# Optimization experiments

Hardware: AMD Instinct MI355X
Metric: run time of the kernel (lower is better)

The kernel has to match this reference:

```python
import jax, jax.numpy as jnp
import numpy as np

B, T, C_FEAT, H = 1024, 256, 512, 256


def setup_inputs() -> dict:
    key = jax.random.key(0)
    ks = jax.random.split(key, 8)
    s_ih = 1.0 / np.sqrt(H)
    return {
        "features": jax.random.normal(ks[0], (B, T, C_FEAT), dtype=jnp.float32),
        "last_coord": jax.random.normal(ks[1], (B, 2), dtype=jnp.float32),
        "W_ih": jax.random.uniform(ks[2], (3 * H, C_FEAT + 2), jnp.float32, -s_ih, s_ih),
        "W_hh": jax.random.uniform(ks[3], (3 * H, H), jnp.float32, -s_ih, s_ih),
        "b_ih": jax.random.uniform(ks[4], (3 * H,), jnp.float32, -s_ih, s_ih),
        "b_hh": jax.random.uniform(ks[5], (3 * H,), jnp.float32, -s_ih, s_ih),
        "W_proj": jax.random.uniform(ks[6], (2, H), jnp.float32, -s_ih, s_ih),
        "b_proj": jax.random.uniform(ks[7], (2,), jnp.float32, -s_ih, s_ih),
    }


def reference(features, last_coord, W_ih, W_hh, b_ih, b_hh, W_proj, b_proj):
    # features: (B, T, C_feat); last_coord: (B, 2)
    Bb, Tt, Cf = features.shape
    Hh = W_hh.shape[1]
    h0 = jnp.zeros((Bb, Hh), dtype=features.dtype)

    def step(carry, feat_t):
        h, coord = carry
        x = jnp.concatenate([feat_t, coord], axis=1)          # (B, C+2)
        gi = x @ W_ih.T + b_ih                                 # (B, 3H)
        gh = h @ W_hh.T + b_hh                                 # (B, 3H)
        i_r, i_z, i_n = jnp.split(gi, 3, axis=1)
        h_r, h_z, h_n = jnp.split(gh, 3, axis=1)
        r = jax.nn.sigmoid(i_r + h_r)
        z = jax.nn.sigmoid(i_z + h_z)
        n = jnp.tanh(i_n + r * h_n)
        h_new = (1.0 - z) * n + z * h                          # PyTorch GRU update
        disp = h_new @ W_proj.T + b_proj                       # (B, 2)
        return (h_new, coord + disp), disp

    feats_t = jnp.swapaxes(features, 0, 1)                     # (T, B, C)
    _, disps = jax.lax.scan(step, (h0, last_coord), feats_t)   # (T, B, 2)
    return jnp.swapaxes(disps, 0, 1)                           # (B, T, 2)
```

## Files before the change

### kernel.cpp

```cpp
#include <hip/hip_runtime.h>
#include <stdint.h>

typedef unsigned short u16;
typedef unsigned int   u32;
typedef __attribute__((ext_vector_type(8))) __bf16 bf16x8;
typedef __attribute__((ext_vector_type(4))) float  f32x4;
typedef __attribute__((ext_vector_type(8))) u16    u16x8;
typedef __attribute__((ext_vector_type(4))) u16    u16x4;
typedef __attribute__((ext_vector_type(2))) u32    u32x2;
typedef __attribute__((ext_vector_type(2))) float  f32x2;

__device__ __forceinline__ u16 f2bf(float f) {
    u32 u = __float_as_uint(f);
    u32 r = (u + 0x7fffu + ((u >> 16) & 1u)) >> 16;
    return (u16)r;
}
__device__ __forceinline__ float bf2f(u16 v) { return __uint_as_float(((u32)v) << 16); }
__device__ __forceinline__ bf16x8 as_bf(u16x8 x) { union { u16x8 a; bf16x8 b; } u; u.a = x; return u.b; }
__device__ __forceinline__ void gload_lds16(const void* g, void* l) {
    __builtin_amdgcn_global_load_lds((const __attribute__((address_space(1))) void*)g,
                                     (__attribute__((address_space(3))) void*)l, 16, 0, 0);
}

__global__ void k_prep(const float* __restrict__ W_ih, const float* __restrict__ W_hh,
                       const float* __restrict__ b_ih, const float* __restrict__ b_hh,
                       u16* __restrict__ Wf, u16* __restrict__ Whh, float* __restrict__ bsum) {
    int i = blockIdx.x * 256 + threadIdx.x;
    if (i < 768 * 512) { int o = i >> 9, k = i & 511; Wf[i] = f2bf(W_ih[o * 514 + k]); }
    if (i < 768 * 256) { Whh[i] = f2bf(W_hh[i]); }
    if (i < 768)       { bsum[i] = b_ih[i] + (i < 512 ? b_hh[i] : 0.f); }
}

__global__ void k_cast(const float* __restrict__ f, u16* __restrict__ o) {
    const size_t N8 = (size_t)262144 * 512 / 8;
    for (size_t i = (size_t)blockIdx.x * 256 + threadIdx.x; i < N8; i += (size_t)gridDim.x * 256) {
        float4 a = ((const float4*)f)[i * 2];
        float4 b = ((const float4*)f)[i * 2 + 1];
        u16x8 v;
        v[0] = f2bf(a.x); v[1] = f2bf(a.y); v[2] = f2bf(a.z); v[3] = f2bf(a.w);
        v[4] = f2bf(b.x); v[5] = f2bf(b.y); v[6] = f2bf(b.z); v[7] = f2bf(b.w);
        ((u16x8*)o)[i] = v;
    }
}

__device__ __forceinline__ void xcd_remap(int& n0, int& m0) {
    int phys = blockIdx.x + blockIdx.y * 6;
    int logical = (phys & 7) * 1536 + (phys >> 3);
    n0 = (logical % 6) * 128;
    m0 = (logical / 6) * 128;
}

__global__ __launch_bounds__(256) void k_gemm(const u16* __restrict__ featbf,
                                              const u16* __restrict__ Wf,
                                              const float* __restrict__ bsum,
                                              float* __restrict__ Gf) {
    __shared__ u16 As[128 * 64];
    __shared__ u16 Bs[128 * 64];
    const int tid = threadIdx.x;
    const int l = tid & 63, wv = tid >> 6;
    const int wr = wv >> 1, wc = wv & 1;
    const int lb = l & 15, lq = l >> 4;
    int n0, m0; xcd_remap(n0, m0);
    const int rl = l >> 3;
    const int c16 = (l & 7) * 16;
    const int sswz = (rl & 7) << 4;

    f32x4 acc[4][4] = {};

    for (int k0 = 0; k0 < 512; k0 += 64) {
        __syncthreads();
#pragma unroll
        for (int i = 0; i < 4; ++i) {
            int ci = wv * 4 + i;
            int r = ci * 8 + rl;
            const char* sa = (const char*)(featbf + (size_t)(m0 + r) * 512) + k0 * 2 + (c16 ^ sswz);
            gload_lds16(sa, (char*)As + ci * 1024);
            const char* sb = (const char*)(Wf + (size_t)(n0 + r) * 512) + k0 * 2 + (c16 ^ sswz);
            gload_lds16(sb, (char*)Bs + ci * 1024);
        }
        __syncthreads();
#pragma unroll
        for (int kc = 0; kc < 2; ++kc) {
            bf16x8 af[4], bfr[4];
#pragma unroll
            for (int mi = 0; mi < 4; ++mi) {
                int row = wr * 64 + mi * 16 + lb;
                af[mi] = *(const bf16x8*)((char*)As + row * 128 + (((kc * 32 + lq * 8) * 2) ^ ((row & 7) << 4)));
            }
#pragma unroll
            for (int ni = 0; ni < 4; ++ni) {
                int row = wc * 64 + ni * 16 + lb;
                bfr[ni] = *(const bf16x8*)((char*)Bs + row * 128 + (((kc * 32 + lq * 8) * 2) ^ ((row & 7) << 4)));
            }
#pragma unroll
            for (int mi = 0; mi < 4; ++mi)
#pragma unroll
                for (int ni = 0; ni < 4; ++ni)
                    acc[mi][ni] = __builtin_amdgcn_mfma_f32_16x16x32_bf16(af[mi], bfr[ni], acc[mi][ni], 0, 0, 0);
        }
    }
#pragma unroll
    for (int ni = 0; ni < 4; ++ni) {
        int o = n0 + wc * 64 + ni * 16 + lb;
        float bi = bsum[o];
#pragma unroll
        for (int mi = 0; mi < 4; ++mi) {
#pragma unroll
            for (int j = 0; j < 4; ++j) {
                int m = m0 + wr * 64 + mi * 16 + lq * 4 + j;
                int bb = m >> 8, tt = m & 255;
                Gf[(size_t)((tt << 10) + bb) * 768 + o] = acc[mi][ni][j] + bi;
            }
        }
    }
}

template<typename ST>
__global__ __launch_bounds__(256) void k_gemm_legacy(const float* __restrict__ feat,
                                                     const u16* __restrict__ Wf,
                                                     const float* __restrict__ bsum,
                                                     ST* __restrict__ Gf) {
    __shared__ u16 As[128 * 64];
    __shared__ u16 Bs[128 * 64];
    const int tid = threadIdx.x;
    const int l = tid & 63, wv = tid >> 6;
    const int wr = wv >> 1, wc = wv & 1;
    const int lb = l & 15, lq = l >> 4;
    int n0, m0; xcd_remap(n0, m0);
    const int srow = tid >> 1, scol = (tid & 1) * 32;

    f32x4 acc[4][4] = {};

    for (int k0 = 0; k0 < 512; k0 += 64) {
        __syncthreads();
        const float* ga = feat + (size_t)(m0 + srow) * 512 + k0 + scol;
        const u16*   gb = Wf + (n0 + srow) * 512 + k0 + scol;
        char* arow = (char*)As + srow * 128;
        char* brow = (char*)Bs + srow * 128;
        const int swz = (srow & 7) << 4;
#pragma unroll
        for (int i = 0; i < 4; ++i) {
            float4 f0 = *(const float4*)(ga + i * 8);
            float4 f1 = *(const float4*)(ga + i * 8 + 4);
            u16x8 v;
            v[0] = f2bf(f0.x); v[1] = f2bf(f0.y); v[2] = f2bf(f0.z); v[3] = f2bf(f0.w);
            v[4] = f2bf(f1.x); v[5] = f2bf(f1.y); v[6] = f2bf(f1.z); v[7] = f2bf(f1.w);
            *(u16x8*)(arow + (((scol + i * 8) * 2) ^ swz)) = v;
            u16x8 w8 = *(const u16x8*)(gb + i * 8);
            *(u16x8*)(brow + (((scol + i * 8) * 2) ^ swz)) = w8;
        }
        __syncthreads();
#pragma unroll
        for (int kc = 0; kc < 2; ++kc) {
            bf16x8 af[4], bfr[4];
#pragma unroll
            for (int mi = 0; mi < 4; ++mi) {
                int row = wr * 64 + mi * 16 + lb;
                af[mi] = *(const bf16x8*)((char*)As + row * 128 + (((kc * 32 + lq * 8) * 2) ^ ((row & 7) << 4)));
            }
#pragma unroll
            for (int ni = 0; ni < 4; ++ni) {
                int row = wc * 64 + ni * 16 + lb;
                bfr[ni] = *(const bf16x8*)((char*)Bs + row * 128 + (((kc * 32 + lq * 8) * 2) ^ ((row & 7) << 4)));
            }
#pragma unroll
            for (int mi = 0; mi < 4; ++mi)
#pragma unroll
                for (int ni = 0; ni < 4; ++ni)
                    acc[mi][ni] = __builtin_amdgcn_mfma_f32_16x16x32_bf16(af[mi], bfr[ni], acc[mi][ni], 0, 0, 0);
        }
    }
#pragma unroll
    for (int ni = 0; ni < 4; ++ni) {
        int o = n0 + wc * 64 + ni * 16 + lb;
        float bi = bsum[o];
#pragma unroll
        for (int mi = 0; mi < 4; ++mi) {
#pragma unroll
            for (int j = 0; j < 4; ++j) {
                int m = m0 + wr * 64 + mi * 16 + lq * 4 + j;
                int bb = m >> 8, tt = m & 255;
                size_t idx = (size_t)((tt << 10) + bb) * 768 + o;
                float v = acc[mi][ni][j] + bi;
                if constexpr (sizeof(ST) == 4) Gf[idx] = v; else Gf[idx] = f2bf(v);
            }
        }
    }
}

template<typename ST>
__global__ __launch_bounds__(512, 2) void k_rnn(const float* __restrict__ lastc,
                                                const float* __restrict__ W_ih,
                                                const float* __restrict__ bhh_g,
                                                const float* __restrict__ Wp,
                                                const float* __restrict__ bp,
                                                const u16* __restrict__ Whh,
                                                const ST* __restrict__ Gf,
                                                float* __restrict__ out) {
    __shared__ u16 Wlds[144 * 512];
    __shared__ u16 hbf[16 * 320];
    __shared__ float wpL[256 * 2];
    __shared__ float coordL[16 * 2];
    __shared__ float dPart[8 * 16 * 2];

    const int tid = threadIdx.x, l = tid & 63, wv = tid >> 6;
    const int lb = l & 15, lq = l >> 4;
    const int bb = blockIdx.x << 4;
    const int swz = (lb & 7) << 4;

    bf16x8 wres[5][3][2];
    bf16x8 wcf[3][2];
    float bhhn[2][4];
#pragma unroll
    for (int g = 0; g < 3; ++g)
#pragma unroll
        for (int ut = 0; ut < 2; ++ut) {
            int row = g * 256 + (2 * wv + ut) * 16 + lb;
#pragma unroll
            for (int kc = 0; kc < 5; ++kc)
                wres[kc][g][ut] = *(const bf16x8*)(Whh + row * 256 + kc * 32 + lq * 8);
            u16x8 cf = {0, 0, 0, 0, 0, 0, 0, 0};
            if (lq == 0) {
                cf[0] = f2bf(W_ih[row * 514 + 512]);
                cf[1] = f2bf(W_ih[row * 514 + 513]);
            }
            wcf[g][ut] = as_bf(cf);
        }
#pragma unroll
    for (int ut = 0; ut < 2; ++ut)
#pragma unroll
        for (int j = 0; j < 4; ++j)
            bhhn[ut][j] = bhh_g[512 + (2 * wv + ut) * 16 + lq * 4 + j];

    for (int i = tid; i < 36864; i += 512) {
        int s = i >> 8, r = i & 255, ll = r >> 2, e2 = r & 3;
        int g = s / 48, rem = s - g * 48, tt = rem / 3, kcs = rem - tt * 3;
        int row = g * 256 + tt * 16 + (ll & 15);
        int k = (5 + kcs) * 32 + (ll >> 4) * 8 + e2 * 2;
        ((u32*)Wlds)[i] = *(const u32*)(Whh + row * 256 + k);
    }
    for (int i = tid; i < 16 * 320 / 2; i += 512) ((u32*)hbf)[i] = 0u;
    if (tid < 256) { wpL[tid * 2] = Wp[tid]; wpL[tid * 2 + 1] = Wp[256 + tid]; }
    float bpc = (tid < 32) ? bp[tid & 1] : 0.f;
    __syncthreads();
    if (tid < 32) {
        int b = tid >> 1, c = tid & 1;
        float cc = lastc[(bb + b) * 2 + c];
        coordL[b * 2 + c] = cc;
        *(u16*)((char*)hbf + b * 640 + 512 + ((c * 2) ^ ((b & 7) << 4))) = f2bf(cc);
    }
    __syncthreads();

    float hreg[2][4] = {};
    float prevD = 0.f;
    const ST* gr = Gf + (size_t)(bb + lb) * 768 + lq * 4;
    const char* hrow = (const char*)hbf + lb * 640;

    for (int t = 0; t < 256; ++t) {
        if (t > 0 && tid < 32)
            out[((size_t)(bb + (tid >> 1)) * 256 + (t - 1)) * 2 + (tid & 1)] = prevD;

        float gf[3][2][4];
#pragma unroll
        for (int g = 0; g < 3; ++g)
#pragma unroll
            for (int ut = 0; ut < 2; ++ut) {
                int off = g * 256 + (2 * wv + ut) * 16;
                if constexpr (sizeof(ST) == 4) {
                    float4 v = *(const float4*)(gr + off);
                    gf[g][ut][0] = v.x; gf[g][ut][1] = v.y; gf[g][ut][2] = v.z; gf[g][ut][3] = v.w;
                } else {
                    u16x4 v = *(const u16x4*)(gr + off);
#pragma unroll
                    for (int j = 0; j < 4; ++j) gf[g][ut][j] = bf2f(v[j]);
                }
            }

        f32x4 acc[3][2] = {};
        f32x4 accC[2] = {};
#pragma unroll
        for (int kc = 0; kc < 5; ++kc) {
            bf16x8 hb = *(const bf16x8*)(hrow + ((kc * 64 + lq * 16) ^ swz));
#pragma unroll
            for (int g = 0; g < 3; ++g)
#pragma unroll
                for (int ut = 0; ut < 2; ++ut)
                    acc[g][ut] = __builtin_amdgcn_mfma_f32_16x16x32_bf16(wres[kc][g][ut], hb, acc[g][ut], 0, 0, 0);
        }
#pragma unroll
        for (int kcs = 0; kcs < 3; ++kcs) {
            bf16x8 hb = *(const bf16x8*)(hrow + (((5 + kcs) * 64 + lq * 16) ^ swz));
#pragma unroll
            for (int g = 0; g < 3; ++g)
#pragma unroll
                for (int ut = 0; ut < 2; ++ut) {
                    int s = (g * 16 + 2 * wv + ut) * 3 + kcs;
                    bf16x8 wl = *(const bf16x8*)((const char*)Wlds + s * 1024 + l * 16);
                    acc[g][ut] = __builtin_amdgcn_mfma_f32_16x16x32_bf16(wl, hb, acc[g][ut], 0, 0, 0);
                }
        }
        {
            bf16x8 hbE = *(const bf16x8*)(hrow + 512 + ((lq * 16) ^ swz));
#pragma unroll
            for (int ut = 0; ut < 2; ++ut) {
                acc[0][ut] = __builtin_amdgcn_mfma_f32_16x16x32_bf16(wcf[0][ut], hbE, acc[0][ut], 0, 0, 0);
                acc[1][ut] = __builtin_amdgcn_mfma_f32_16x16x32_bf16(wcf[1][ut], hbE, acc[1][ut], 0, 0, 0);
                accC[ut]   = __builtin_amdgcn_mfma_f32_16x16x32_bf16(wcf[2][ut], hbE, accC[ut],   0, 0, 0);
            }
        }
        __syncthreads();

        float pd0 = 0.f, pd1 = 0.f;
#pragma unroll
        for (int ut = 0; ut < 2; ++ut) {
            int ub = (2 * wv + ut) * 16 + lq * 4;
            float4 wpa = *(const float4*)(wpL + ub * 2);
            float4 wpb = *(const float4*)(wpL + ub * 2 + 4);
            u16 hpk[4];
#pragma unroll
            for (int j = 0; j < 4; ++j) {
                float r = 1.f / (1.f + __expf(-(gf[0][ut][j] + acc[0][ut][j])));
                float z = 1.f / (1.f + __expf(-(gf[1][ut][j] + acc[1][ut][j])));
                float ghn = acc[2][ut][j] + bhhn[ut][j];
                float xn = gf[2][ut][j] + accC[ut][j] + r * ghn;
                float e = __expf(-2.f * fabsf(xn));
                float th = (1.f - e) / (1.f + e);
                th = (xn >= 0.f) ? th : -th;
                float hn = (1.f - z) * th + z * hreg[ut][j];
                hreg[ut][j] = hn;
                float w0 = (j == 0) ? wpa.x : (j == 1) ? wpa.z : (j == 2) ? wpb.x : wpb.z;
                float w1 = (j == 0) ? wpa.y : (j == 1) ? wpa.w : (j == 2) ? wpb.y : wpb.w;
                pd0 += w0 * hn;
                pd1 += w1 * hn;
                hpk[j] = f2bf(hn);
            }
            u32x2 pv;
            pv.x = (u32)hpk[0] | ((u32)hpk[1] << 16);
            pv.y = (u32)hpk[2] | ((u32)hpk[3] << 16);
            *(u32x2*)((char*)hbf + lb * 640 + ((ub * 2) ^ swz)) = pv;
        }
        pd0 += __shfl_xor(pd0, 16); pd0 += __shfl_xor(pd0, 32);
        pd1 += __shfl_xor(pd1, 16); pd1 += __shfl_xor(pd1, 32);
        if (l < 16) { dPart[(wv * 16 + l) * 2] = pd0; dPart[(wv * 16 + l) * 2 + 1] = pd1; }
        __syncthreads();

        if (tid < 32) {
            int b = tid >> 1, c = tid & 1;
            float d = bpc;
#pragma unroll
            for (int w8 = 0; w8 < 8; ++w8) d += dPart[(w8 * 16 + b) * 2 + c];
            prevD = d;
            float nc = coordL[b * 2 + c] + d;
            coordL[b * 2 + c] = nc;
            *(u16*)((char*)hbf + b * 640 + 512 + ((c * 2) ^ ((b & 7) << 4))) = f2bf(nc);
        }
        __syncthreads();
        gr += (size_t)1024 * 768;
    }
    if (tid < 32)
        out[((size_t)(bb + (tid >> 1)) * 256 + 255) * 2 + (tid & 1)] = prevD;
}

extern "C" void kernel_launch(void* const* d_in, const int* in_sizes, int n_in,
                              void* d_out, int out_size, void* d_ws, size_t ws_size,
                              hipStream_t stream) {
    const float* feat   = (const float*)d_in[0];
    const float* lastc  = (const float*)d_in[1];
    const float* W_ih   = (const float*)d_in[2];
    const float* W_hh   = (const float*)d_in[3];
    const float* b_ih   = (const float*)d_in[4];
    const float* b_hh   = (const float*)d_in[5];
    const float* W_proj = (const float*)d_in[6];
    const float* b_proj = (const float*)d_in[7];
    float* out = (float*)d_out;

    char* ws = (char*)d_ws;
    u16*   Wf    = (u16*)ws;
    u16*   Whh   = (u16*)(ws + 786432);
    float* bsum  = (float*)(ws + 786432 + 393216);
    const size_t off_fb = 786432 + 393216 + 3072;
    u16*   featbf = (u16*)(ws + off_fb);
    const size_t off_gf_full = off_fb + (size_t)262144 * 512 * 2;
    const size_t need_full  = off_gf_full + (size_t)262144 * 768 * 4;
    const size_t need_tier2 = off_fb + (size_t)262144 * 768 * 4;

    k_prep<<<1536, 256, 0, stream>>>(W_ih, W_hh, b_ih, b_hh, Wf, Whh, bsum);

    if (ws_size >= need_full) {
        float* Gf = (float*)(ws + off_gf_full);
        k_cast<<<16384, 256, 0, stream>>>(feat, featbf);
        k_gemm<<<dim3(6, 2048), 256, 0, stream>>>(featbf, Wf, bsum, Gf);
        k_rnn<float><<<64, 512, 0, stream>>>(lastc, W_ih, b_hh, W_proj, b_proj, Whh, Gf, out);
    } else if (ws_size >= need_tier2) {
        float* Gf = (float*)(ws + off_fb);
        k_gemm_legacy<float><<<dim3(6, 2048), 256, 0, stream>>>(feat, Wf, bsum, Gf);
        k_rnn<float><<<64, 512, 0, stream>>>(lastc, W_ih, b_hh, W_proj, b_proj, Whh, Gf, out);
    } else {
        u16* Gf = (u16*)(ws + off_fb);
        k_gemm_legacy<u16><<<dim3(6, 2048), 256, 0, stream>>>(feat, Wf, bsum, Gf);
        k_rnn<u16><<<64, 512, 0, stream>>>(lastc, W_ih, b_hh, W_proj, b_proj, Whh, Gf, out);
    }
}
```

Measured before the change: 1.511 ms.

## Double RNN block to 16 waves, split weights across regs/LDS/global, stage gates via LDS

The recurrent kernel now runs 1024 threads (16 waves) per block, so each wave owns one 16-unit tile per gate instead of two. This halves the per-wave MFMA chain on the serial timestep path. W_hh k-chunks 0-4 stay in registers, chunks 6-7 move to LDS, and chunk 5 is re-read from global/L2 every step. Precomputed input gates are prefetched into LDS with async global_load_lds at the start of each step, hiding load latency behind the MFMAs. The cost is heavier barriers across 16 waves, a larger projection reduction, and an extra global weight load per step.

```diff
diff --git a/kernel.cpp b/kernel.cpp
--- a/kernel.cpp
+++ b/kernel.cpp
@@ -8,7 +8,6 @@
 typedef __attribute__((ext_vector_type(8))) u16    u16x8;
 typedef __attribute__((ext_vector_type(4))) u16    u16x4;
 typedef __attribute__((ext_vector_type(2))) u32    u32x2;
-typedef __attribute__((ext_vector_type(2))) float  f32x2;
 
 __device__ __forceinline__ u16 f2bf(float f) {
     u32 u = __float_as_uint(f);
@@ -189,57 +188,54 @@
 }
 
 template<typename ST>
-__global__ __launch_bounds__(512, 2) void k_rnn(const float* __restrict__ lastc,
-                                                const float* __restrict__ W_ih,
-                                                const float* __restrict__ bhh_g,
-                                                const float* __restrict__ Wp,
-                                                const float* __restrict__ bp,
-                                                const u16* __restrict__ Whh,
-                                                const ST* __restrict__ Gf,
-                                                float* __restrict__ out) {
-    __shared__ u16 Wlds[144 * 512];
+__global__ __launch_bounds__(1024, 4) void k_rnn(const float* __restrict__ lastc,
+                                                 const float* __restrict__ W_ih,
+                                                 const float* __restrict__ bhh_g,
+                                                 const float* __restrict__ Wp,
+                                                 const float* __restrict__ bp,
+                                                 const u16* __restrict__ Whh,
+                                                 const ST* __restrict__ Gf,
+                                                 float* __restrict__ out) {
+    __shared__ u16 Wlds[96 * 512];
+    __shared__ __align__(16) char GfL[16 * 3120];
     __shared__ u16 hbf[16 * 320];
     __shared__ float wpL[256 * 2];
     __shared__ float coordL[16 * 2];
-    __shared__ float dPart[8 * 16 * 2];
+    __shared__ float dPart[16 * 16 * 2];
 
     const int tid = threadIdx.x, l = tid & 63, wv = tid >> 6;
     const int lb = l & 15, lq = l >> 4;
     const int bb = blockIdx.x << 4;
     const int swz = (lb & 7) << 4;
 
-    bf16x8 wres[5][3][2];
-    bf16x8 wcf[3][2];
-    float bhhn[2][4];
-#pragma unroll
-    for (int g = 0; g < 3; ++g)
-#pragma unroll
-        for (int ut = 0; ut < 2; ++ut) {
-            int row = g * 256 + (2 * wv + ut) * 16 + lb;
-#pragma unroll
-            for (int kc = 0; kc < 5; ++kc)
-                wres[kc][g][ut] = *(const bf16x8*)(Whh + row * 256 + kc * 32 + lq * 8);
-            u16x8 cf = {0, 0, 0, 0, 0, 0, 0, 0};
-            if (lq == 0) {
-                cf[0] = f2bf(W_ih[row * 514 + 512]);
-                cf[1] = f2bf(W_ih[row * 514 + 513]);
-            }
-            wcf[g][ut] = as_bf(cf);
-        }
-#pragma unroll
-    for (int ut = 0; ut < 2; ++ut)
-#pragma unroll
-        for (int j = 0; j < 4; ++j)
-            bhhn[ut][j] = bhh_g[512 + (2 * wv + ut) * 16 + lq * 4 + j];
-
-    for (int i = tid; i < 36864; i += 512) {
+    bf16x8 wres[5][3];
+    bf16x8 wcf[3];
+    float bhhn[4];
+#pragma unroll
+    for (int g = 0; g < 3; ++g) {
+        int row = g * 256 + wv * 16 + lb;
+#pragma unroll
+        for (int kc = 0; kc < 5; ++kc)
+            wres[kc][g] = *(const bf16x8*)(Whh + row * 256 + kc * 32 + lq * 8);
+        u16x8 cf = {0, 0, 0, 0, 0, 0, 0, 0};
+        if (lq == 0) {
+            cf[0] = f2bf(W_ih[row * 514 + 512]);
+            cf[1] = f2bf(W_ih[row * 514 + 513]);
+        }
+        wcf[g] = as_bf(cf);
+    }
+#pragma unroll
+    for (int j = 0; j < 4; ++j)
+        bhhn[j] = bhh_g[512 + wv * 16 + lq * 4 + j];
+
+    for (int i = tid; i < 24576; i += 1024) {
         int s = i >> 8, r = i & 255, ll = r >> 2, e2 = r & 3;
-        int g = s / 48, rem = s - g * 48, tt = rem / 3, kcs = rem - tt * 3;
-        int row = g * 256 + tt * 16 + (ll & 15);
-        int k = (5 + kcs) * 32 + (ll >> 4) * 8 + e2 * 2;
+        int g = s >> 5, rem = s & 31, tt2 = rem >> 1, kcs = rem & 1;
+        int row = g * 256 + tt2 * 16 + (ll & 15);
+        int k = (6 + kcs) * 32 + (ll >> 4) * 8 + e2 * 2;
         ((u32*)Wlds)[i] = *(const u32*)(Whh + row * 256 + k);
     }
-    for (int i = tid; i < 16 * 320 / 2; i += 512) ((u32*)hbf)[i] = 0u;
+    for (int i = tid; i < 2560; i += 1024) ((u32*)hbf)[i] = 0u;
     if (tid < 256) { wpL[tid * 2] = Wp[tid]; wpL[tid * 2 + 1] = Wp[256 + tid]; }
     float bpc = (tid < 32) ? bp[tid & 1] : 0.f;
     __syncthreads();
@@ -251,89 +247,98 @@
     }
     __syncthreads();
 
-    float hreg[2][4] = {};
+    float hreg[4] = {};
     float prevD = 0.f;
-    const ST* gr = Gf + (size_t)(bb + lb) * 768 + lq * 4;
     const char* hrow = (const char*)hbf + lb * 640;
+    const u16* w5base = Whh + (size_t)(wv * 16 + lb) * 256 + 160 + lq * 8;
 
     for (int t = 0; t < 256; ++t) {
         if (t > 0 && tid < 32)
             out[((size_t)(bb + (tid >> 1)) * 256 + (t - 1)) * 2 + (tid & 1)] = prevD;
 
-        float gf[3][2][4];
+        if constexpr (sizeof(ST) == 4) {
+            const char* gsrc = (const char*)Gf + (size_t)t * 3145728 + (size_t)(bb + wv) * 3072;
+#pragma unroll
+            for (int i = 0; i < 3; ++i)
+                gload_lds16(gsrc + i * 1024 + l * 16, GfL + wv * 3120 + i * 1024);
+        }
+        bf16x8 w5[3];
 #pragma unroll
         for (int g = 0; g < 3; ++g)
-#pragma unroll
-            for (int ut = 0; ut < 2; ++ut) {
-                int off = g * 256 + (2 * wv + ut) * 16;
-                if constexpr (sizeof(ST) == 4) {
-                    float4 v = *(const float4*)(gr + off);
-                    gf[g][ut][0] = v.x; gf[g][ut][1] = v.y; gf[g][ut][2] = v.z; gf[g][ut][3] = v.w;
-                } else {
-                    u16x4 v = *(const u16x4*)(gr + off);
-#pragma unroll
-                    for (int j = 0; j < 4; ++j) gf[g][ut][j] = bf2f(v[j]);
-                }
-            }
-
-        f32x4 acc[3][2] = {};
-        f32x4 accC[2] = {};
+            w5[g] = *(const bf16x8*)(w5base + g * 65536);
+
+        f32x4 acc[3] = {};
+        f32x4 accC = {};
 #pragma unroll
         for (int kc = 0; kc < 5; ++kc) {
             bf16x8 hb = *(const bf16x8*)(hrow + ((kc * 64 + lq * 16) ^ swz));
 #pragma unroll
             for (int g = 0; g < 3; ++g)
-#pragma unroll
-                for (int ut = 0; ut < 2; ++ut)
-                    acc[g][ut] = __builtin_amdgcn_mfma_f32_16x16x32_bf16(wres[kc][g][ut], hb, acc[g][ut], 0, 0, 0);
-        }
-#pragma unroll
-        for (int kcs = 0; kcs < 3; ++kcs) {
-            bf16x8 hb = *(const bf16x8*)(hrow + (((5 + kcs) * 64 + lq * 16) ^ swz));
+                acc[g] = __builtin_amdgcn_mfma_f32_16x16x32_bf16(wres[kc][g], hb, acc[g], 0, 0, 0);
+        }
+#pragma unroll
+        for (int kcs = 0; kcs < 2; ++kcs) {
+            bf16x8 hb = *(const bf16x8*)(hrow + (((6 + kcs) * 64 + lq * 16) ^ swz));
+#pragma unroll
+            for (int g = 0; g < 3; ++g) {
+                int s = (g * 16 + wv) * 2 + kcs;
+                bf16x8 wl = *(const bf16x8*)((const char*)Wlds + s * 1024 + l * 16);
+                acc[g] = __builtin_amdgcn_mfma_f32_16x16x32_bf16(wl, hb, acc[g], 0, 0, 0);
+            }
+        }
+        {
+            bf16x8 hb5 = *(const bf16x8*)(hrow + ((5 * 64 + lq * 16) ^ swz));
 #pragma unroll
             for (int g = 0; g < 3; ++g)
-#pragma unroll
-                for (int ut = 0; ut < 2; ++ut) {
-                    int s = (g * 16 + 2 * wv + ut) * 3 + kcs;
-                    bf16x8 wl = *(const bf16x8*)((const char*)Wlds + s * 1024 + l * 16);
-                    acc[g][ut] = __builtin_amdgcn_mfma_f32_16x16x32_bf16(wl, hb, acc[g][ut], 0, 0, 0);
-                }
+                acc[g] = __builtin_amdgcn_mfma_f32_16x16x32_bf16(w5[g], hb5, acc[g], 0, 0, 0);
         }
         {
             bf16x8 hbE = *(const bf16x8*)(hrow + 512 + ((lq * 16) ^ swz));
-#pragma unroll
-            for (int ut = 0; ut < 2; ++ut) {
-                acc[0][ut] = __builtin_amdgcn_mfma_f32_16x16x32_bf16(wcf[0][ut], hbE, acc[0][ut], 0, 0, 0);
-                acc[1][ut] = __builtin_amdgcn_mfma_f32_16x16x32_bf16(wcf[1][ut], hbE, acc[1][ut], 0, 0, 0);
-                accC[ut]   = __builtin_amdgcn_mfma_f32_16x16x32_bf16(wcf[2][ut], hbE, accC[ut],   0, 0, 0);
-            }
-        }
-        __syncthreads();
-
+            acc[0] = __builtin_amdgcn_mfma_f32_16x16x32_bf16(wcf[0], hbE, acc[0], 0, 0, 0);
+            acc[1] = __builtin_amdgcn_mfma_f32_16x16x32_bf16(wcf[1], hbE, acc[1], 0, 0, 0);
+            accC   = __builtin_amdgcn_mfma_f32_16x16x32_bf16(wcf[2], hbE, accC,   0, 0, 0);
+        }
+        __syncthreads();
+
+        const int ub = wv * 16 + lq * 4;
+        float4 wpa = *(const float4*)(wpL + ub * 2);
+        float4 wpb = *(const float4*)(wpL + ub * 2 + 4);
+        float gfv[3][4];
+        if constexpr (sizeof(ST) == 4) {
+#pragma unroll
+            for (int g = 0; g < 3; ++g) {
+                float4 v = *(const float4*)(GfL + lb * 3120 + (g * 256 + ub) * 4);
+                gfv[g][0] = v.x; gfv[g][1] = v.y; gfv[g][2] = v.z; gfv[g][3] = v.w;
+            }
+        } else {
+            const ST* gr = Gf + ((size_t)t * 1024 + bb + lb) * 768 + ub;
+#pragma unroll
+            for (int g = 0; g < 3; ++g) {
+                u16x4 v = *(const u16x4*)(gr + g * 256);
+#pragma unroll
+                for (int j = 0; j < 4; ++j) gfv[g][j] = bf2f(v[j]);
+            }
+        }
         float pd0 = 0.f, pd1 = 0.f;
-#pragma unroll
-        for (int ut = 0; ut < 2; ++ut) {
-            int ub = (2 * wv + ut) * 16 + lq * 4;
-            float4 wpa = *(const float4*)(wpL + ub * 2);
-            float4 wpb = *(const float4*)(wpL + ub * 2 + 4);
-            u16 hpk[4];
-#pragma unroll
-            for (int j = 0; j < 4; ++j) {
-                float r = 1.f / (1.f + __expf(-(gf[0][ut][j] + acc[0][ut][j])));
-                float z = 1.f / (1.f + __expf(-(gf[1][ut][j] + acc[1][ut][j])));
-                float ghn = acc[2][ut][j] + bhhn[ut][j];
-                float xn = gf[2][ut][j] + accC[ut][j] + r * ghn;
-                float e = __expf(-2.f * fabsf(xn));
-                float th = (1.f - e) / (1.f + e);
-                th = (xn >= 0.f) ? th : -th;
-                float hn = (1.f - z) * th + z * hreg[ut][j];
-                hreg[ut][j] = hn;
-                float w0 = (j == 0) ? wpa.x : (j == 1) ? wpa.z : (j == 2) ? wpb.x : wpb.z;
-                float w1 = (j == 0) ? wpa.y : (j == 1) ? wpa.w : (j == 2) ? wpb.y : wpb.w;
-                pd0 += w0 * hn;
-                pd1 += w1 * hn;
-                hpk[j] = f2bf(hn);
-            }
+        u16 hpk[4];
+#pragma unroll
+        for (int j = 0; j < 4; ++j) {
+            float r = 1.f / (1.f + __expf(-(gfv[0][j] + acc[0][j])));
+            float z = 1.f / (1.f + __expf(-(gfv[1][j] + acc[1][j])));
+            float ghn = acc[2][j] + bhhn[j];
+            float xn = gfv[2][j] + accC[j] + r * ghn;
+            float e = __expf(-2.f * fabsf(xn));
+            float th = (1.f - e) / (1.f + e);
+            th = (xn >= 0.f) ? th : -th;
+            float hn = (1.f - z) * th + z * hreg[j];
+            hreg[j] = hn;
+            float w0 = (j == 0) ? wpa.x : (j == 1) ? wpa.z : (j == 2) ? wpb.x : wpb.z;
+            float w1 = (j == 0) ? wpa.y : (j == 1) ? wpa.w : (j == 2) ? wpb.y : wpb.w;
+            pd0 += w0 * hn;
+            pd1 += w1 * hn;
+            hpk[j] = f2bf(hn);
+        }
+        {
             u32x2 pv;
             pv.x = (u32)hpk[0] | ((u32)hpk[1] << 16);
             pv.y = (u32)hpk[2] | ((u32)hpk[3] << 16);
@@ -348,14 +353,13 @@
             int b = tid >> 1, c = tid & 1;
             float d = bpc;
 #pragma unroll
-            for (int w8 = 0; w8 < 8; ++w8) d += dPart[(w8 * 16 + b) * 2 + c];
+            for (int w = 0; w < 16; ++w) d += dPart[(w * 16 + b) * 2 + c];
             prevD = d;
             float nc = coordL[b * 2 + c] + d;
             coordL[b * 2 + c] = nc;
             *(u16*)((char*)hbf + b * 640 + 512 + ((c * 2) ^ ((b & 7) << 4))) = f2bf(nc);
         }
         __syncthreads();
-        gr += (size_t)1024 * 768;
     }
     if (tid < 32)
         out[((size_t)(bb + (tid >> 1)) * 256 + 255) * 2 + (tid & 1)] = prevD;
@@ -390,14 +394,14 @@
         float* Gf = (float*)(ws + off_gf_full);
         k_cast<<<16384, 256, 0, stream>>>(feat, featbf);
         k_gemm<<<dim3(6, 2048), 256, 0, stream>>>(featbf, Wf, bsum, Gf);
-        k_rnn<float><<<64, 512, 0, stream>>>(lastc, W_ih, b_hh, W_proj, b_proj, Whh, Gf, out);
+        k_rnn<float><<<64, 1024, 0, stream>>>(lastc, W_ih, b_hh, W_proj, b_proj, Whh, Gf, out);
     } else if (ws_size >= need_tier2) {
         float* Gf = (float*)(ws + off_fb);
         k_gemm_legacy<float><<<dim3(6, 2048), 256, 0, stream>>>(feat, Wf, bsum, Gf);
-        k_rnn<float><<<64, 512, 0, stream>>>(lastc, W_ih, b_hh, W_proj, b_proj, Whh, Gf, out);
+        k_rnn<float><<<64, 1024, 0, stream>>>(lastc, W_ih, b_hh, W_proj, b_proj, Whh, Gf, out);
     } else {
         u16* Gf = (u16*)(ws + off_fb);
         k_gemm_legacy<u16><<<dim3(6, 2048), 256, 0, stream>>>(feat, Wf, bsum, Gf);
-        k_rnn<u16><<<64, 512, 0, stream>>>(lastc, W_ih, b_hh, W_proj, b_proj, Whh, Gf, out);
-    }
-}
+        k_rnn<u16><<<64, 1024, 0, stream>>>(lastc, W_ih, b_hh, W_proj, b_proj, Whh, Gf, out);
+    }
+}
```

Result: slower. 2.155 ms (+42.6%).

## Stage input-gate rows through LDS via async loads and stream one W_hh chunk from global

Applied to the files above, without the earlier changes.

In the recurrent kernel, the per-step precomputed input-gate values are now copied into LDS with asynchronous global-to-LDS loads that all waves issue at the start of each step, then read from LDS in the gate epilogue. This replaces the per-thread strided float4 global gathers that had to finish before the MFMA chain began. To make room in LDS, one of the three LDS-resident W_hh k-chunks is dropped and re-read from global (L2) every step as a register fragment. The change trades extra per-step global weight traffic and register pressure for better latency hiding of the gate-input loads.

```diff
diff --git a/kernel.cpp b/kernel.cpp
--- a/kernel.cpp
+++ b/kernel.cpp
@@ -8,7 +8,6 @@
 typedef __attribute__((ext_vector_type(8))) u16    u16x8;
 typedef __attribute__((ext_vector_type(4))) u16    u16x4;
 typedef __attribute__((ext_vector_type(2))) u32    u32x2;
-typedef __attribute__((ext_vector_type(2))) float  f32x2;
 
 __device__ __forceinline__ u16 f2bf(float f) {
     u32 u = __float_as_uint(f);
@@ -197,7 +196,8 @@
                                                 const u16* __restrict__ Whh,
                                                 const ST* __restrict__ Gf,
                                                 float* __restrict__ out) {
-    __shared__ u16 Wlds[144 * 512];
+    __shared__ u16 Wlds[96 * 512];
+    __shared__ __align__(16) char GfL[16 * 3104];
     __shared__ u16 hbf[16 * 320];
     __shared__ float wpL[256 * 2];
     __shared__ float coordL[16 * 2];
@@ -232,11 +232,11 @@
         for (int j = 0; j < 4; ++j)
             bhhn[ut][j] = bhh_g[512 + (2 * wv + ut) * 16 + lq * 4 + j];
 
-    for (int i = tid; i < 36864; i += 512) {
+    for (int i = tid; i < 24576; i += 512) {
         int s = i >> 8, r = i & 255, ll = r >> 2, e2 = r & 3;
-        int g = s / 48, rem = s - g * 48, tt = rem / 3, kcs = rem - tt * 3;
-        int row = g * 256 + tt * 16 + (ll & 15);
-        int k = (5 + kcs) * 32 + (ll >> 4) * 8 + e2 * 2;
+        int g = s >> 5, rem = s & 31, tt2 = rem >> 1, kcs = rem & 1;
+        int row = g * 256 + tt2 * 16 + (ll & 15);
+        int k = (6 + kcs) * 32 + (ll >> 4) * 8 + e2 * 2;
         ((u32*)Wlds)[i] = *(const u32*)(Whh + row * 256 + k);
     }
     for (int i = tid; i < 16 * 320 / 2; i += 512) ((u32*)hbf)[i] = 0u;
@@ -253,28 +253,27 @@
 
     float hreg[2][4] = {};
     float prevD = 0.f;
-    const ST* gr = Gf + (size_t)(bb + lb) * 768 + lq * 4;
     const char* hrow = (const char*)hbf + lb * 640;
 
     for (int t = 0; t < 256; ++t) {
         if (t > 0 && tid < 32)
             out[((size_t)(bb + (tid >> 1)) * 256 + (t - 1)) * 2 + (tid & 1)] = prevD;
 
-        float gf[3][2][4];
+        if constexpr (sizeof(ST) == 4) {
+            const char* gsrc = (const char*)Gf + ((size_t)t * 1024 + bb + 2 * wv) * 3072 + l * 16;
+            char* gdst = GfL + (2 * wv) * 3104;
+#pragma unroll
+            for (int bi = 0; bi < 2; ++bi)
+#pragma unroll
+                for (int c = 0; c < 3; ++c)
+                    gload_lds16(gsrc + bi * 3072 + c * 1024, gdst + bi * 3104 + c * 1024);
+        }
+        bf16x8 w5[3][2];
 #pragma unroll
         for (int g = 0; g < 3; ++g)
 #pragma unroll
-            for (int ut = 0; ut < 2; ++ut) {
-                int off = g * 256 + (2 * wv + ut) * 16;
-                if constexpr (sizeof(ST) == 4) {
-                    float4 v = *(const float4*)(gr + off);
-                    gf[g][ut][0] = v.x; gf[g][ut][1] = v.y; gf[g][ut][2] = v.z; gf[g][ut][3] = v.w;
-                } else {
-                    u16x4 v = *(const u16x4*)(gr + off);
-#pragma unroll
-                    for (int j = 0; j < 4; ++j) gf[g][ut][j] = bf2f(v[j]);
-                }
-            }
+            for (int ut = 0; ut < 2; ++ut)
+                w5[g][ut] = *(const bf16x8*)(Whh + (size_t)(g * 256 + (2 * wv + ut) * 16 + lb) * 256 + 160 + lq * 8);
 
         f32x4 acc[3][2] = {};
         f32x4 accC[2] = {};
@@ -288,16 +287,24 @@
                     acc[g][ut] = __builtin_amdgcn_mfma_f32_16x16x32_bf16(wres[kc][g][ut], hb, acc[g][ut], 0, 0, 0);
         }
 #pragma unroll
-        for (int kcs = 0; kcs < 3; ++kcs) {
-            bf16x8 hb = *(const bf16x8*)(hrow + (((5 + kcs) * 64 + lq * 16) ^ swz));
+        for (int kcs = 0; kcs < 2; ++kcs) {
+            bf16x8 hb = *(const bf16x8*)(hrow + (((6 + kcs) * 64 + lq * 16) ^ swz));
 #pragma unroll
             for (int g = 0; g < 3; ++g)
 #pragma unroll
                 for (int ut = 0; ut < 2; ++ut) {
-                    int s = (g * 16 + 2 * wv + ut) * 3 + kcs;
+                    int s = (g * 16 + 2 * wv + ut) * 2 + kcs;
                     bf16x8 wl = *(const bf16x8*)((const char*)Wlds + s * 1024 + l * 16);
                     acc[g][ut] = __builtin_amdgcn_mfma_f32_16x16x32_bf16(wl, hb, acc[g][ut], 0, 0, 0);
                 }
+        }
+        {
+            bf16x8 hb5 = *(const bf16x8*)(hrow + ((5 * 64 + lq * 16) ^ swz));
+#pragma unroll
+            for (int g = 0; g < 3; ++g)
+#pragma unroll
+                for (int ut = 0; ut < 2; ++ut)
+                    acc[g][ut] = __builtin_amdgcn_mfma_f32_16x16x32_bf16(w5[g][ut], hb5, acc[g][ut], 0, 0, 0);
         }
         {
             bf16x8 hbE = *(const bf16x8*)(hrow + 512 + ((lq * 16) ^ swz));
@@ -316,13 +323,29 @@
             int ub = (2 * wv + ut) * 16 + lq * 4;
             float4 wpa = *(const float4*)(wpL + ub * 2);
             float4 wpb = *(const float4*)(wpL + ub * 2 + 4);
+            float gfv[3][4];
+            if constexpr (sizeof(ST) == 4) {
+#pragma unroll
+                for (int g = 0; g < 3; ++g) {
+                    float4 v = *(const float4*)(GfL + lb * 3104 + (g * 256 + ub) * 4);
+                    gfv[g][0] = v.x; gfv[g][1] = v.y; gfv[g][2] = v.z; gfv[g][3] = v.w;
+                }
+            } else {
+                const ST* gr = Gf + ((size_t)t * 1024 + bb + lb) * 768 + ub;
+#pragma unroll
+                for (int g = 0; g < 3; ++g) {
+                    u16x4 v = *(const u16x4*)(gr + g * 256);
+#pragma unroll
+                    for (int j = 0; j < 4; ++j) gfv[g][j] = bf2f(v[j]);
+                }
+            }
             u16 hpk[4];
 #pragma unroll
             for (int j = 0; j < 4; ++j) {
-                float r = 1.f / (1.f + __expf(-(gf[0][ut][j] + acc[0][ut][j])));
-                float z = 1.f / (1.f + __expf(-(gf[1][ut][j] + acc[1][ut][j])));
+                float r = 1.f / (1.f + __expf(-(gfv[0][j] + acc[0][ut][j])));
+                float z = 1.f / (1.f + __expf(-(gfv[1][j] + acc[1][ut][j])));
                 float ghn = acc[2][ut][j] + bhhn[ut][j];
-                float xn = gf[2][ut][j] + accC[ut][j] + r * ghn;
+                float xn = gfv[2][j] + accC[ut][j] + r * ghn;
                 float e = __expf(-2.f * fabsf(xn));
                 float th = (1.f - e) / (1.f + e);
                 th = (xn >= 0.f) ? th : -th;
@@ -355,7 +378,6 @@
             *(u16*)((char*)hbf + b * 640 + 512 + ((c * 2) ^ ((b & 7) << 4))) = f2bf(nc);
         }
         __syncthreads();
-        gr += (size_t)1024 * 768;
     }
     if (tid < 32)
         out[((size_t)(bb + (tid >> 1)) * 256 + 255) * 2 + (tid & 1)] = prevD;
```

New measurement: 1.700 ms. 1.13x slower.
